# Performance work log

Measured on AMD Instinct MI355X. Metric: run time of the kernel, lower is better.

Reference implementation:

```python
import jax, jax.numpy as jnp
import numpy as np

N_NODES = 50000
N_EDGES = 800000
IN_DIM = 89
HID = 128


def gcn_conv(x, src, dst, deg_inv_sqrt, W, b):
    # PyG GCNConv: x' = D^{-1/2} (A + I) D^{-1/2} (x W) + b
    h = x @ W  # [N, F_out]
    norm = deg_inv_sqrt[src] * deg_inv_sqrt[dst]  # per-edge norm [E]
    msgs = h[src] * norm[:, None]  # gather + scale [E, F_out]
    agg = jax.ops.segment_sum(msgs, dst, num_segments=x.shape[0])
    # self-loop contribution: norm = deg_inv_sqrt[i]^2
    agg = agg + h * (deg_inv_sqrt * deg_inv_sqrt)[:, None]
    return agg + b


def setup_inputs() -> dict:
    key = jax.random.key(0)
    k1, k2, k3, k4, k5, k6 = jax.random.split(key, 6)
    x = jax.random.normal(k1, (N_NODES, IN_DIM), dtype=jnp.float32)
    edge_index = jax.random.randint(k2, (2, N_EDGES), 0, N_NODES, dtype=jnp.int64)
    # Glorot-style init for GCN weights
    W1 = jax.random.normal(k3, (IN_DIM, HID), dtype=jnp.float32) * (1.0 / np.sqrt(IN_DIM))
    b1 = jnp.zeros((HID,), dtype=jnp.float32)
    W2 = jax.random.normal(k4, (HID, HID), dtype=jnp.float32) * (1.0 / np.sqrt(HID))
    b2 = jnp.zeros((HID,), dtype=jnp.float32)
    return {"x": x, "edge_index": edge_index, "W1": W1, "b1": b1, "W2": W2, "b2": b2}


def reference(x, edge_index, W1, b1, W2, b2):
    src = edge_index[0]
    dst = edge_index[1]
    n = x.shape[0]
    # degree of A + I: 1 (self loop) + in-degree
    deg = 1.0 + jax.ops.segment_sum(jnp.ones((src.shape[0],), x.dtype), dst, num_segments=n)
    deg_inv_sqrt = jax.lax.rsqrt(deg)
    h = jax.nn.relu(gcn_conv(x, src, dst, deg_inv_sqrt, W1, b1))
    h = jax.nn.relu(gcn_conv(h, src, dst, deg_inv_sqrt, W2, b2))
    return (h, edge_index)
```

## Files before the change

kernel.cpp:

```cpp
#include <hip/hip_runtime.h>
#include <hip/hip_bf16.h>


#define HID 128
#define KIN 89
#define KP 128
#define BSH 7
#define BNODES 128
#define MAXBUCK 512
#define NPB 128
#define P4CAP 3072
#define LDSPAD 136

typedef __attribute__((ext_vector_type(8))) short bf16x8;
typedef __attribute__((ext_vector_type(4))) float f32x4;

static __device__ inline float2 unpack_bf16(unsigned v) {
    union { unsigned u; float f; } lo, hi;
    lo.u = v << 16;
    hi.u = v & 0xFFFF0000u;
    return make_float2(lo.f, hi.f);
}

static __device__ inline unsigned pack_bf16(float a, float b) {
    __hip_bfloat162 h = __float22bfloat162_rn(make_float2(a, b));
    return *reinterpret_cast<unsigned*>(&h);
}

static __device__ inline unsigned short f2bf(float v) {
    __hip_bfloat16 h = __float2bfloat16(v);
    return *reinterpret_cast<unsigned short*>(&h);
}

__global__ __launch_bounds__(256) void p1_kernel(
    const int* __restrict__ ei, float* __restrict__ outE,
    int* __restrict__ histG,
    const float* __restrict__ W1, unsigned short* __restrict__ W1t,
    const float* __restrict__ W2, unsigned short* __restrict__ W2t,
    int E, int nbuck)
{
    __shared__ int h[MAXBUCK];
    const int tid = threadIdx.x, blk = blockIdx.x;
    const int* src = ei;
    const int* dst = ei + E;
    for (int b = tid; b < nbuck; b += 256) h[b] = 0;

    int tg = blk * 256 + tid;
    if (tg < HID * KP) {
        int n = tg / KP, k = tg % KP;
        W1t[tg] = f2bf(k < KIN ? W1[(size_t)k * HID + n] : 0.0f);
    } else {
        int t2 = tg - HID * KP;
        if (t2 < HID * HID) {
            int n = t2 / HID, k = t2 % HID;
            W2t[t2] = f2bf(W2[(size_t)k * HID + n]);
        }
    }
    __syncthreads();

    const int chunk = (E + NPB - 1) / NPB;
    const int beg = blk * chunk, end = min(beg + chunk, E);
    for (int i = beg + tid; i < end; i += 256) {
        int d = dst[i];
        atomicAdd(&h[d >> BSH], 1);
        outE[i] = (float)src[i];
        outE[E + i] = (float)d;
    }
    __syncthreads();
    for (int b = tid; b < nbuck; b += 256) histG[b * NPB + blk] = h[b];
}

__global__ __launch_bounds__(NPB) void p2a_kernel(
    int* __restrict__ histG, int* __restrict__ totals)
{
    __shared__ int wsum[NPB / 64];
    const int b = blockIdx.x, tid = threadIdx.x, lane = tid & 63, wid = tid >> 6;
    int c = histG[b * NPB + tid];
    int s = c;
#pragma unroll
    for (int off = 1; off < 64; off <<= 1) {
        int t = __shfl_up(s, off, 64);
        if (lane >= off) s += t;
    }
    if (lane == 63) wsum[wid] = s;
    __syncthreads();
    if (tid == 0) {
        int a = 0;
#pragma unroll
        for (int w = 0; w < NPB / 64; ++w) { int t = wsum[w]; wsum[w] = a; a += t; }
    }
    __syncthreads();
    int excl = wsum[wid] + s - c;
    histG[b * NPB + tid] = excl;
    if (tid == NPB - 1) totals[b] = excl + c;
}

static __device__ inline void scan_totals2(const int* __restrict__ totals,
                                           int* __restrict__ sexcl,
                                           int* __restrict__ wsum,
                                           int nbuck, int tid)
{
    const int lane = tid & 63, wid = tid >> 6;
    const int i0 = 2 * tid, i1 = 2 * tid + 1;
    int t0 = (i0 < nbuck) ? totals[i0] : 0;
    int t1 = (i1 < nbuck) ? totals[i1] : 0;
    int p = t0 + t1;
    int s = p;
#pragma unroll
    for (int off = 1; off < 64; off <<= 1) {
        int t = __shfl_up(s, off, 64);
        if (lane >= off) s += t;
    }
    if (lane == 63) wsum[wid] = s;
    __syncthreads();
    if (tid == 0) {
        int a = 0;
#pragma unroll
        for (int w = 0; w < 4; ++w) { int t = wsum[w]; wsum[w] = a; a += t; }
    }
    __syncthreads();
    int excl = wsum[wid] + s - p;
    sexcl[i0] = excl;
    sexcl[i1] = excl + t0;
}

__global__ __launch_bounds__(256) void p3_part_kernel(
    const int* __restrict__ ei, const int* __restrict__ histG,
    const int* __restrict__ totals, unsigned* __restrict__ ebuf,
    int E, int nbuck)
{
    __shared__ int cur[MAXBUCK];
    __shared__ int wsum[4];
    const int tid = threadIdx.x, blk = blockIdx.x;
    const int* src = ei;
    const int* dst = ei + E;
    scan_totals2(totals, cur, wsum, nbuck, tid);
    __syncthreads();
    for (int b = tid; b < nbuck; b += 256) cur[b] += histG[b * NPB + blk];
    const int chunk = (E + NPB - 1) / NPB;
    const int beg = blk * chunk, end = min(beg + chunk, E);
    __syncthreads();
    for (int i = beg + tid; i < end; i += 256) {
        int d = dst[i];
        int b = d >> BSH;
        int pos = atomicAdd(&cur[b], 1);
        ebuf[pos] = ((unsigned)(d & (BNODES - 1)) << 16) | (unsigned)src[i];
    }
}

__global__ __launch_bounds__(256) void p4_sort_kernel(
    const unsigned* __restrict__ ebuf, const int* __restrict__ totals,
    unsigned short* __restrict__ csr, int* __restrict__ rowptr,
    float* __restrict__ dis, int N, int E, int nbuck)
{
    __shared__ int counts[BNODES];
    __shared__ int cursor[BNODES];
    __shared__ int sbase[MAXBUCK];
    __shared__ int wsum[4];
    __shared__ int w2[2];
    __shared__ unsigned short staging[P4CAP];
    const int b = blockIdx.x, tid = threadIdx.x, lane = tid & 63, wid = tid >> 6;

    scan_totals2(totals, sbase, wsum, nbuck, tid);
    __syncthreads();
    const int gbase = sbase[b];
    const int cnt = totals[b];

    if (tid < BNODES) counts[tid] = 0;
    __syncthreads();
    for (int i = tid; i < cnt; i += 256)
        atomicAdd(&counts[ebuf[gbase + i] >> 16], 1);
    __syncthreads();

    int c = 0, s = 0;
    if (tid < BNODES) {
        c = counts[tid];
        s = c;
#pragma unroll
        for (int off = 1; off < 64; off <<= 1) {
            int t = __shfl_up(s, off, 64);
            if (lane >= off) s += t;
        }
        if (lane == 63) w2[wid] = s;
    }
    __syncthreads();
    if (tid == 0) { int t = w2[0]; w2[0] = 0; w2[1] = t; }
    __syncthreads();
    if (tid < BNODES) {
        int excl = w2[wid] + s - c;
        cursor[tid] = excl;
        int node = b * BNODES + tid;
        if (node < N) {
            rowptr[node] = gbase + excl;
            dis[node] = rsqrtf(1.0f + (float)c);
        }
    }
    if (b == 0 && tid == 0) rowptr[N] = E;
    __syncthreads();

    if (cnt <= P4CAP) {
        for (int i = tid; i < cnt; i += 256) {
            unsigned v = ebuf[gbase + i];
            int pos = atomicAdd(&cursor[v >> 16], 1);
            staging[pos] = (unsigned short)(v & 0xFFFFu);
        }
        __syncthreads();
        for (int i = tid; i < cnt; i += 256)
            csr[gbase + i] = staging[i];
    } else {
        for (int i = tid; i < cnt; i += 256) {
            unsigned v = ebuf[gbase + i];
            int pos = atomicAdd(&cursor[v >> 16], 1);
            csr[gbase + pos] = (unsigned short)(v & 0xFFFFu);
        }
    }
}

__global__ __launch_bounds__(256) void xconv_kernel(
    const float* __restrict__ X, const float* __restrict__ dis,
    unsigned* __restrict__ Xhs, int N)
{
    int t = blockIdx.x * 256 + threadIdx.x;
    if (t >= N * (KP / 2)) return;
    int n = t / (KP / 2), c = t % (KP / 2);
    float d = dis[n];
    const float* xr = X + (size_t)n * KIN;
    float a = (2 * c     < KIN) ? d * xr[2 * c]     : 0.0f;
    float b = (2 * c + 1 < KIN) ? d * xr[2 * c + 1] : 0.0f;
    Xhs[t] = pack_bf16(a, b);
}

template<bool LAYER1>
__global__ __launch_bounds__(256) void fused_kernel(
    const uint4* __restrict__ rows, const int* __restrict__ rowptr,
    const unsigned short* __restrict__ csr,
    const unsigned short* __restrict__ Wt, const float* __restrict__ bias,
    const float* __restrict__ dis, void* __restrict__ outp, int N)
{
    __shared__ unsigned short lds_a[64][LDSPAD];
    const int tid  = threadIdx.x;
    const int wave = tid >> 6;
    const int lane = tid & 63;
    const int sub  = (lane >> 4) & 3;
    const int sl   = lane & 15;
    const int blk0 = blockIdx.x * 64;

#pragma unroll
    for (int p = 0; p < 4; ++p) {
        const int lrow = wave * 16 + p * 4 + sub;
        const int node = blk0 + lrow;
        const bool valid = node < N;
        const int cn = valid ? node : N - 1;

        uint4 sv = rows[(size_t)cn * 16 + sl];
        float a0, a1, a2, a3, a4, a5, a6, a7;
        {
            float2 q;
            q = unpack_bf16(sv.x); a0 = q.x; a1 = q.y;
            q = unpack_bf16(sv.y); a2 = q.x; a3 = q.y;
            q = unpack_bf16(sv.z); a4 = q.x; a5 = q.y;
            q = unpack_bf16(sv.w); a6 = q.x; a7 = q.y;
        }

        int beg = rowptr[cn];
        int end = valid ? rowptr[cn + 1] : beg;
        int j = beg;
        for (; j + 4 <= end; j += 4) {
            int r0 = csr[j], r1 = csr[j + 1], r2 = csr[j + 2], r3 = csr[j + 3];
            uint4 v0 = rows[(size_t)r0 * 16 + sl];
            uint4 v1 = rows[(size_t)r1 * 16 + sl];
            uint4 v2 = rows[(size_t)r2 * 16 + sl];
            uint4 v3 = rows[(size_t)r3 * 16 + sl];
            float2 q;
            q = unpack_bf16(v0.x); a0 += q.x; a1 += q.y;
            q = unpack_bf16(v0.y); a2 += q.x; a3 += q.y;
            q = unpack_bf16(v0.z); a4 += q.x; a5 += q.y;
            q = unpack_bf16(v0.w); a6 += q.x; a7 += q.y;
            q = unpack_bf16(v1.x); a0 += q.x; a1 += q.y;
            q = unpack_bf16(v1.y); a2 += q.x; a3 += q.y;
            q = unpack_bf16(v1.z); a4 += q.x; a5 += q.y;
            q = unpack_bf16(v1.w); a6 += q.x; a7 += q.y;
            q = unpack_bf16(v2.x); a0 += q.x; a1 += q.y;
            q = unpack_bf16(v2.y); a2 += q.x; a3 += q.y;
            q = unpack_bf16(v2.z); a4 += q.x; a5 += q.y;
            q = unpack_bf16(v2.w); a6 += q.x; a7 += q.y;
            q = unpack_bf16(v3.x); a0 += q.x; a1 += q.y;
            q = unpack_bf16(v3.y); a2 += q.x; a3 += q.y;
            q = unpack_bf16(v3.z); a4 += q.x; a5 += q.y;
            q = unpack_bf16(v3.w); a6 += q.x; a7 += q.y;
        }
        for (; j < end; ++j) {
            int r = csr[j];
            uint4 v = rows[(size_t)r * 16 + sl];
            float2 q;
            q = unpack_bf16(v.x); a0 += q.x; a1 += q.y;
            q = unpack_bf16(v.y); a2 += q.x; a3 += q.y;
            q = unpack_bf16(v.z); a4 += q.x; a5 += q.y;
            q = unpack_bf16(v.w); a6 += q.x; a7 += q.y;
        }

        uint4 pk = make_uint4(pack_bf16(a0, a1), pack_bf16(a2, a3),
                              pack_bf16(a4, a5), pack_bf16(a6, a7));
        *(uint4*)&lds_a[lrow][sl * 8] = pk;
    }
    __syncthreads();

    const int m    = lane & 15;
    const int quad = lane >> 4;
    const int node = blk0 + wave * 16 + m;

    f32x4 acc[8];
#pragma unroll
    for (int t = 0; t < 8; ++t) acc[t] = (f32x4){0.0f, 0.0f, 0.0f, 0.0f};

    const unsigned short* arp = &lds_a[wave * 16 + m][0];

#pragma unroll
    for (int c = 0; c < KP / 32; ++c) {
        const int k0 = c * 32 + quad * 8;
        bf16x8 nv = *(const bf16x8*)(arp + k0);
#pragma unroll
        for (int t = 0; t < 8; ++t) {
            bf16x8 wv = *(const bf16x8*)(Wt + (size_t)(t * 16 + m) * KP + k0);
            acc[t] = __builtin_amdgcn_mfma_f32_16x16x32_bf16(wv, nv, acc[t], 0, 0, 0);
        }
    }

    if (node < N) {
        const float dv = dis[node];
#pragma unroll
        for (int t = 0; t < 8; ++t) {
            const int col0 = t * 16 + quad * 4;
            float4 bb = *(const float4*)&bias[col0];
            float r0 = fmaxf(fmaf(dv, acc[t][0], bb.x), 0.0f);
            float r1 = fmaxf(fmaf(dv, acc[t][1], bb.y), 0.0f);
            float r2 = fmaxf(fmaf(dv, acc[t][2], bb.z), 0.0f);
            float r3 = fmaxf(fmaf(dv, acc[t][3], bb.w), 0.0f);
            if (LAYER1) {
                uint2 u;
                u.x = pack_bf16(r0 * dv, r1 * dv);
                u.y = pack_bf16(r2 * dv, r3 * dv);
                *(uint2*)((unsigned short*)outp + (size_t)node * HID + col0) = u;
            } else {
                float4 r = make_float4(r0, r1, r2, r3);
                *(float4*)((float*)outp + (size_t)node * HID + col0) = r;
            }
        }
    }
}


static inline char* wsal(char*& p, size_t n) {
    uintptr_t q = ((uintptr_t)p + 255) & ~(uintptr_t)255;
    char* r = (char*)q;
    p = r + n;
    return r;
}

extern "C" void kernel_launch(void* const* d_in, const int* in_sizes, int n_in,
                              void* d_out, int out_size, void* d_ws, size_t ws_size,
                              hipStream_t stream) {
    const float* x  = (const float*)d_in[0];
    const int*   ei = (const int*)d_in[1];
    const float* W1 = (const float*)d_in[2];
    const float* b1 = (const float*)d_in[3];
    const float* W2 = (const float*)d_in[4];
    const float* b2 = (const float*)d_in[5];

    const int N = in_sizes[0] / KIN;
    const int E = in_sizes[1] / 2;
    const int nbuck = (N + BNODES - 1) >> BSH;

    float* out  = (float*)d_out;
    float* outH = out;
    float* outE = out + (size_t)N * HID;

    char* ws = (char*)d_ws;
    int*            histG  = (int*)wsal(ws, (size_t)MAXBUCK * NPB * 4);
    int*            totals = (int*)wsal(ws, MAXBUCK * 4);
    int*            rowptr = (int*)wsal(ws, (size_t)(N + 1) * 4);
    float*          dis    = (float*)wsal(ws, (size_t)N * 4);
    unsigned*       ebuf   = (unsigned*)wsal(ws, (size_t)E * 4);
    unsigned short* csr    = (unsigned short*)wsal(ws, (size_t)E * 2);
    unsigned*       Xhs    = (unsigned*)wsal(ws, (size_t)N * (KP / 2) * 4);
    unsigned short* g2h    = (unsigned short*)wsal(ws, (size_t)N * HID * 2);
    unsigned short* W1t    = (unsigned short*)wsal(ws, (size_t)HID * KP * 2);
    unsigned short* W2t    = (unsigned short*)wsal(ws, (size_t)HID * HID * 2);

    p1_kernel<<<NPB, 256, 0, stream>>>(ei, outE, histG, W1, W1t, W2, W2t, E, nbuck);
    p2a_kernel<<<nbuck, NPB, 0, stream>>>(histG, totals);
    p3_part_kernel<<<NPB, 256, 0, stream>>>(ei, histG, totals, ebuf, E, nbuck);
    p4_sort_kernel<<<nbuck, 256, 0, stream>>>(ebuf, totals, csr, rowptr, dis,
                                              N, E, nbuck);
    xconv_kernel<<<(N * (KP / 2) + 255) / 256, 256, 0, stream>>>(x, dis, Xhs, N);

    const int ngf = (N + 63) / 64;

    fused_kernel<true><<<ngf, 256, 0, stream>>>(
        (const uint4*)Xhs, rowptr, csr, W1t, b1, dis, g2h, N);

    fused_kernel<false><<<ngf, 256, 0, stream>>>(
        (const uint4*)g2h, rowptr, csr, W2t, b2, dis, outH, N);
}
```

Measured before the change: 220.7 us.

## Shrink fused GCN block to 16 nodes and split output columns across waves

Each block of the fused aggregate+GEMM kernel now handles 16 nodes instead of 64. Each wave gathers 4 node rows once rather than looping over 16. In the MFMA stage the four waves split the 128 output columns, two 16-column tiles each, instead of each wave computing all 8 tiles for its own 16 nodes. This gives four times as many blocks, lower register and LDS use, and more parallelism for the latency-bound gather. The cost is that weight tiles are reloaded across four times as many blocks, and per-block sync and launch overhead grows.

```diff
diff --git a/kernel.cpp b/kernel.cpp
--- a/kernel.cpp
+++ b/kernel.cpp
@@ -237,17 +237,16 @@
     const unsigned short* __restrict__ Wt, const float* __restrict__ bias,
     const float* __restrict__ dis, void* __restrict__ outp, int N)
 {
-    __shared__ unsigned short lds_a[64][LDSPAD];
+    __shared__ unsigned short lds_a[16][LDSPAD];
     const int tid  = threadIdx.x;
     const int wave = tid >> 6;
     const int lane = tid & 63;
     const int sub  = (lane >> 4) & 3;
     const int sl   = lane & 15;
-    const int blk0 = blockIdx.x * 64;
-
-#pragma unroll
-    for (int p = 0; p < 4; ++p) {
-        const int lrow = wave * 16 + p * 4 + sub;
+    const int blk0 = blockIdx.x * 16;
+
+    {
+        const int lrow = wave * 4 + sub;
         const int node = blk0 + lrow;
         const bool valid = node < N;
         const int cn = valid ? node : N - 1;
@@ -307,35 +306,36 @@
 
     const int m    = lane & 15;
     const int quad = lane >> 4;
-    const int node = blk0 + wave * 16 + m;
-
-    f32x4 acc[8];
-#pragma unroll
-    for (int t = 0; t < 8; ++t) acc[t] = (f32x4){0.0f, 0.0f, 0.0f, 0.0f};
-
-    const unsigned short* arp = &lds_a[wave * 16 + m][0];
+    const int node = blk0 + m;
+
+    f32x4 acc[2];
+    acc[0] = (f32x4){0.0f, 0.0f, 0.0f, 0.0f};
+    acc[1] = (f32x4){0.0f, 0.0f, 0.0f, 0.0f};
+
+    const unsigned short* arp = &lds_a[m][0];
 
 #pragma unroll
     for (int c = 0; c < KP / 32; ++c) {
         const int k0 = c * 32 + quad * 8;
         bf16x8 nv = *(const bf16x8*)(arp + k0);
 #pragma unroll
-        for (int t = 0; t < 8; ++t) {
+        for (int t2 = 0; t2 < 2; ++t2) {
+            const int t = wave * 2 + t2;
             bf16x8 wv = *(const bf16x8*)(Wt + (size_t)(t * 16 + m) * KP + k0);
-            acc[t] = __builtin_amdgcn_mfma_f32_16x16x32_bf16(wv, nv, acc[t], 0, 0, 0);
+            acc[t2] = __builtin_amdgcn_mfma_f32_16x16x32_bf16(wv, nv, acc[t2], 0, 0, 0);
         }
     }
 
     if (node < N) {
         const float dv = dis[node];
 #pragma unroll
-        for (int t = 0; t < 8; ++t) {
-            const int col0 = t * 16 + quad * 4;
+        for (int t2 = 0; t2 < 2; ++t2) {
+            const int col0 = (wave * 2 + t2) * 16 + quad * 4;
             float4 bb = *(const float4*)&bias[col0];
-            float r0 = fmaxf(fmaf(dv, acc[t][0], bb.x), 0.0f);
-            float r1 = fmaxf(fmaf(dv, acc[t][1], bb.y), 0.0f);
-            float r2 = fmaxf(fmaf(dv, acc[t][2], bb.z), 0.0f);
-            float r3 = fmaxf(fmaf(dv, acc[t][3], bb.w), 0.0f);
+            float r0 = fmaxf(fmaf(dv, acc[t2][0], bb.x), 0.0f);
+            float r1 = fmaxf(fmaf(dv, acc[t2][1], bb.y), 0.0f);
+            float r2 = fmaxf(fmaf(dv, acc[t2][2], bb.z), 0.0f);
+            float r3 = fmaxf(fmaf(dv, acc[t2][3], bb.w), 0.0f);
             if (LAYER1) {
                 uint2 u;
                 u.x = pack_bf16(r0 * dv, r1 * dv);
@@ -394,7 +394,7 @@
                                               N, E, nbuck);
     xconv_kernel<<<(N * (KP / 2) + 255) / 256, 256, 0, stream>>>(x, dis, Xhs, N);
 
-    const int ngf = (N + 63) / 64;
+    const int ngf = (N + 15) / 16;
 
     fused_kernel<true><<<ngf, 256, 0, stream>>>(
         (const uint4*)Xhs, rowptr, csr, W1t, b1, dis, g2h, N);
```

New measurement: 203.8 us. 1.08x faster.
